# Performance work log

Measured on AMD Instinct MI355X. Metric: run time of the kernel, lower is better.

The kernel has to match this reference:

```python
import jax, jax.numpy as jnp
import numpy as np
from jax import lax

B, C_IN, C_OUT, T, D = 8, 32, 32, 2048, 32
L = T + 1  # max_timesteps=2048 is even -> pos length 2049


def setup_inputs() -> dict:
    key = jax.random.key(0)
    ks = jax.random.split(key, 8)
    x = jax.random.normal(ks[0], (B, C_IN, T), dtype=jnp.float32)
    # register_buffer pos_rel = linspace(-1, 1, L) with shape (1, 1, L)
    pos_rel = jnp.linspace(-1.0, 1.0, L, dtype=jnp.float32).reshape(1, 1, L)
    # SIREN init: first Conv1d weight ~ U(-1,1); later layers ~ U(-val,val), val=sqrt(6/in)/omega_0 (omega_0=1)
    w1 = jax.random.uniform(ks[1], (D, 1), jnp.float32, -1.0, 1.0)
    b1 = jax.random.uniform(ks[2], (D,), jnp.float32, -1.0, 1.0)
    val2 = float(np.sqrt(6.0 / D))
    w2 = jax.random.uniform(ks[3], (D, D), jnp.float32, -val2, val2)
    b2 = jax.random.uniform(ks[4], (D,), jnp.float32, -val2, val2)
    w3 = jax.random.uniform(ks[5], (C_OUT * C_IN, D), jnp.float32, -val2, val2)
    b3 = jax.random.uniform(ks[6], (C_OUT * C_IN,), jnp.float32, -val2, val2)
    bias = jax.random.normal(ks[7], (C_OUT,), dtype=jnp.float32)
    return {"x": x, "pos_rel": pos_rel, "w1": w1, "b1": b1, "w2": w2,
            "b2": b2, "w3": w3, "b3": b3, "bias": bias}


def reference(x, pos_rel, w1, b1, w2, b2, w3, b3, bias):
    # Kernel network (all kernel_size-1 convs == pointwise matmuls over positions).
    # Note: Sine.forward is sin(linear(x)); omega_0 param is unused in forward.
    p = pos_rel[0]                                   # (1, L)
    h = jnp.sin(w1 @ p + b1[:, None])                # (D, L)
    h = jnp.sin(w2 @ h + b2[:, None])                # (D, L)
    k = w3 @ h + b3[:, None]                         # (C_OUT*C_IN, L)
    kernel = k.reshape(C_OUT, C_IN, L)               # conv weight (O, I, K)
    # Causal left-padding with K-1 zeros, then VALID cross-correlation (torch conv1d semantics).
    xp = jnp.pad(x, ((0, 0), (0, 0), (L - 1, 0)))    # (B, C_IN, T+L-1)
    out = lax.conv_general_dilated(xp, kernel, window_strides=(1,), padding='VALID',
                                   dimension_numbers=('NCH', 'OIH', 'NCH'))
    return out + bias[None, :, None]                 # (B, C_OUT, T)
```

## Files before the change

kernel.cpp:

```cpp
#include <hip/hip_runtime.h>
#include <hip/hip_bf16.h>

#define BATCH 8
#define TLEN 2048
#define PADR 256
#define XT_ROWS (TLEN + PADR + 64)
#define GT_BYTES (2048*1024*2)
#define XT_BYTES (BATCH*XT_ROWS*32*2)
#define PART_OFF ((GT_BYTES + XT_BYTES + 255) & ~255)
#define JOBS_PER_B 144
#define NJOBS (BATCH*JOBS_PER_B)

using short8 = __attribute__((ext_vector_type(8))) short;
using f32x4  = __attribute__((ext_vector_type(4))) float;

typedef __attribute__((address_space(3))) char lds_char;
typedef __attribute__((address_space(1))) const char g_char;
static __device__ __forceinline__ void gload16(const void* g, void* l) {
    __builtin_amdgcn_global_load_lds((g_char*)g, (lds_char*)l, 16, 0, 0);
}

__global__ __launch_bounds__(256) void prep_kernel(
        const float* __restrict__ pos, const float* __restrict__ w1,
        const float* __restrict__ b1, const float* __restrict__ w2,
        const float* __restrict__ b2, const float* __restrict__ w3,
        const float* __restrict__ b3, const float* __restrict__ x,
        __hip_bfloat16* __restrict__ Gt, __hip_bfloat16* __restrict__ xT) {
    __shared__ float ot[128][65];
    int tid = threadIdx.x;
    if (blockIdx.x < 256) {
        int dblk = blockIdx.x >> 3, oblk = blockIdx.x & 7;
        int l  = tid & 63;
        int wu = __builtin_amdgcn_readfirstlane(tid >> 6);
        int d  = dblk*64 + l;
        float p = pos[2048 - d];
        float t1[32], h2[32];
        #pragma unroll
        for (int k = 0; k < 32; ++k) t1[k] = sinf(w1[k]*p + b1[k]);
        #pragma unroll
        for (int j = 0; j < 32; ++j) {
            float s0 = 0.f, s1 = 0.f;
            #pragma unroll
            for (int k = 0; k < 16; ++k) {
                s0 += w2[j*32 + k]      * t1[k];
                s1 += w2[j*32 + 16 + k] * t1[16 + k];
            }
            h2[j] = sinf(b2[j] + s0 + s1);
        }
        int obase = oblk*128 + wu*32;
        for (int ji = 0; ji < 32; ++ji) {
            int oi = obase + ji;
            float s0 = 0.f, s1 = 0.f;
            #pragma unroll
            for (int k = 0; k < 16; ++k) {
                s0 += w3[oi*32 + k]      * h2[k];
                s1 += w3[oi*32 + 16 + k] * h2[16 + k];
            }
            ot[wu*32 + ji][l] = b3[oi] + s0 + s1;
        }
        __syncthreads();
        #pragma unroll
        for (int it = 0; it < 32; ++it) {
            int e  = it*256 + tid;
            int dl = e >> 7, jq = e & 127;
            Gt[(size_t)(dblk*64 + dl)*1024 + oblk*128 + jq] = __float2bfloat16(ot[jq][dl]);
        }
    } else {
        int blk = blockIdx.x - 256;
        int b = blk >> 5;
        int c = blk & 31;
        int t0 = c * 64;
        #pragma unroll
        for (int r = 0; r < 8; ++r) {
            int i  = r*4 + (tid >> 6);
            int tl = tid & 63;
            ot[i][tl] = x[((size_t)(b*32 + i))*TLEN + t0 + tl];
        }
        __syncthreads();
        #pragma unroll
        for (int r = 0; r < 8; ++r) {
            int idx = r*256 + tid;
            int tl = idx >> 5, i = idx & 31;
            xT[((size_t)(b*XT_ROWS + PADR + t0 + tl))*32 + i] = __float2bfloat16(ot[i][tl]);
        }
        if (c == 0) {
            for (int idx = tid; idx < PADR*32; idx += 256)
                xT[(size_t)b*XT_ROWS*32 + idx] = __float2bfloat16(0.0f);
        }
        if (c == 1) {
            for (int idx = tid; idx < 64*32; idx += 256)
                xT[((size_t)b*XT_ROWS + PADR + TLEN)*32 + idx] = __float2bfloat16(0.0f);
        }
    }
}

#define MFMA8(A0,A1,A2,A3,B0,B1)                                                  \
    acc[0][0] = __builtin_amdgcn_mfma_f32_16x16x32_bf16(A0, B0, acc[0][0], 0,0,0); \
    acc[0][1] = __builtin_amdgcn_mfma_f32_16x16x32_bf16(A0, B1, acc[0][1], 0,0,0); \
    acc[1][0] = __builtin_amdgcn_mfma_f32_16x16x32_bf16(A1, B0, acc[1][0], 0,0,0); \
    acc[1][1] = __builtin_amdgcn_mfma_f32_16x16x32_bf16(A1, B1, acc[1][1], 0,0,0); \
    acc[2][0] = __builtin_amdgcn_mfma_f32_16x16x32_bf16(A2, B0, acc[2][0], 0,0,0); \
    acc[2][1] = __builtin_amdgcn_mfma_f32_16x16x32_bf16(A2, B1, acc[2][1], 0,0,0); \
    acc[3][0] = __builtin_amdgcn_mfma_f32_16x16x32_bf16(A3, B0, acc[3][0], 0,0,0); \
    acc[3][1] = __builtin_amdgcn_mfma_f32_16x16x32_bf16(A3, B1, acc[3][1], 0,0,0);

__global__ __launch_bounds__(256) void conv_mfma(const __hip_bfloat16* __restrict__ GtB,
                                                 const __hip_bfloat16* __restrict__ xTB,
                                                 float* __restrict__ partial) {
    __shared__ short8 lds_a[320*4];
    __shared__ short8 lds_b[2][1024];
    int tid  = threadIdx.x;
    int lane = tid & 63;
    int wu   = __builtin_amdgcn_readfirstlane(tid >> 6);
    int jid  = blockIdx.x;
    int b    = jid / JOBS_PER_B;
    int r    = jid - b * JOBS_PER_B;
    int J = (int)((sqrtf(2.0f*r + 1.0f) - 1.0f) * 0.5f);
    while (2*(J+1)*(J+2) <= r) ++J;
    while (2*J*(J+1) > r) --J;
    int S  = r - 2*J*(J+1);
    int d0 = 64*S;

    const short8* xs = (const short8*)xTB;
    int g0 = b*XT_ROWS + PADR + 256*J - 64*S - 63;
    #pragma unroll
    for (int c = 0; c < 5; ++c) {
        int lr   = c*64 + (tid >> 2);
        int slot = tid & 3;
        lds_a[lr*4 + (slot ^ ((lr >> 1) & 3))] = xs[(size_t)(g0 + lr)*4 + slot];
    }
    const char* gB = (const char*)GtB + (size_t)d0*2048;
    {
        const char* src = gB + wu*4096 + lane*16;
        char*       dst = (char*)(&lds_b[0][0]) + wu*4096;
        #pragma unroll
        for (int i = 0; i < 4; ++i) gload16(src + i*1024, dst + i*1024);
    }
    __syncthreads();

    int l15 = lane & 15, l4 = lane >> 4;
    int r0 = 63 + 64*wu + l15;

    f32x4 acc[4][2];
    const f32x4 zero = {0.f, 0.f, 0.f, 0.f};
    #pragma unroll
    for (int mt = 0; mt < 4; ++mt) { acc[mt][0] = zero; acc[mt][1] = zero; }

    for (int p = 0; p < 8; ++p) {
        if (p < 7) {
            const char* src = gB + (p+1)*16384 + wu*4096 + lane*16;
            char*       dst = (char*)(&lds_b[(p+1)&1][0]) + wu*4096;
            #pragma unroll
            for (int i = 0; i < 4; ++i) gload16(src + i*1024, dst + i*1024);
        }
        const short8* bb = &lds_b[p&1][0];
        #pragma unroll
        for (int q = 0; q < 8; ++q) {
            short8 bv0 = bb[q*128 + l15*4 + l4];
            short8 bv1 = bb[q*128 + l15*4 + l4 + 64];
            int ai = r0*4 + (l4 ^ ((r0 >> 1) & 3));
            short8 a0 = lds_a[ai], a1 = lds_a[ai+64], a2 = lds_a[ai+128], a3 = lds_a[ai+192];
            r0--;
            MFMA8(a0, a1, a2, a3, bv0, bv1)
        }
        __syncthreads();
    }

    float* pw = partial + (size_t)jid * 8192;
    #pragma unroll
    for (int no = 0; no < 2; ++no)
        #pragma unroll
        for (int mt = 0; mt < 4; ++mt) {
            int addr = (16*no + l15)*256 + 64*wu + 16*mt + l4*4;
            *reinterpret_cast<f32x4*>(pw + addr) = acc[mt][no];
        }
}

__global__ void reduce_out(const float* __restrict__ partial, const float* __restrict__ bias,
                           float* __restrict__ out) {
    int gid = blockIdx.x * 256 + threadIdx.x;
    int tl = gid & 255;
    int J  = (gid >> 8) & 7;
    int o  = (gid >> 11) & 31;
    int b  = gid >> 16;
    int jid = b*JOBS_PER_B + 2*J*(J+1);
    int cnt = 4*(J+1);
    const float* p = partial + (size_t)jid*8192 + o*256 + tl;
    float s0 = 0.f, s1 = 0.f, s2 = 0.f, s3 = 0.f;
    for (int sg = 0; sg < cnt; sg += 4) {
        s0 += p[(size_t)sg*8192];
        s1 += p[(size_t)(sg+1)*8192];
        s2 += p[(size_t)(sg+2)*8192];
        s3 += p[(size_t)(sg+3)*8192];
    }
    out[((size_t)(b*32 + o))*TLEN + 256*J + tl] = bias[o] + ((s0 + s1) + (s2 + s3));
}

extern "C" void kernel_launch(void* const* d_in, const int* in_sizes, int n_in,
                              void* d_out, int out_size, void* d_ws, size_t ws_size,
                              hipStream_t stream) {
    const float* x    = (const float*)d_in[0];
    const float* pos  = (const float*)d_in[1];
    const float* w1   = (const float*)d_in[2];
    const float* b1   = (const float*)d_in[3];
    const float* w2   = (const float*)d_in[4];
    const float* b2   = (const float*)d_in[5];
    const float* w3   = (const float*)d_in[6];
    const float* b3   = (const float*)d_in[7];
    const float* bias = (const float*)d_in[8];
    float* out = (float*)d_out;

    char* ws = (char*)d_ws;
    __hip_bfloat16* Gt = (__hip_bfloat16*)ws;
    __hip_bfloat16* xT = (__hip_bfloat16*)(ws + GT_BYTES);
    float* partial     = (float*)(ws + PART_OFF);

    hipLaunchKernelGGL(prep_kernel, dim3(512),   dim3(256), 0, stream,
                       pos, w1, b1, w2, b2, w3, b3, x, Gt, xT);
    hipLaunchKernelGGL(conv_mfma,   dim3(NJOBS), dim3(256), 0, stream, Gt, xT, partial);
    hipLaunchKernelGGL(reduce_out,  dim3(2048),  dim3(256), 0, stream, partial, bias, out);
}
```

Before: 151.1 us.

## Replace partial-sum buffer and reduce kernel with atomic accumulation into output

```diff
diff --git a/kernel.cpp b/kernel.cpp
--- a/kernel.cpp
+++ b/kernel.cpp
@@ -7,7 +7,6 @@
 #define XT_ROWS (TLEN + PADR + 64)
 #define GT_BYTES (2048*1024*2)
 #define XT_BYTES (BATCH*XT_ROWS*32*2)
-#define PART_OFF ((GT_BYTES + XT_BYTES + 255) & ~255)
 #define JOBS_PER_B 144
 #define NJOBS (BATCH*JOBS_PER_B)
 
@@ -25,7 +24,9 @@
         const float* __restrict__ b1, const float* __restrict__ w2,
         const float* __restrict__ b2, const float* __restrict__ w3,
         const float* __restrict__ b3, const float* __restrict__ x,
-        __hip_bfloat16* __restrict__ Gt, __hip_bfloat16* __restrict__ xT) {
+        const float* __restrict__ bias,
+        __hip_bfloat16* __restrict__ Gt, __hip_bfloat16* __restrict__ xT,
+        float* __restrict__ out) {
     __shared__ float ot[128][65];
     int tid = threadIdx.x;
     if (blockIdx.x < 256) {
@@ -65,7 +66,7 @@
             int dl = e >> 7, jq = e & 127;
             Gt[(size_t)(dblk*64 + dl)*1024 + oblk*128 + jq] = __float2bfloat16(ot[jq][dl]);
         }
-    } else {
+    } else if (blockIdx.x < 512) {
         int blk = blockIdx.x - 256;
         int b = blk >> 5;
         int c = blk & 31;
@@ -91,6 +92,13 @@
             for (int idx = tid; idx < 64*32; idx += 256)
                 xT[((size_t)b*XT_ROWS + PADR + TLEN)*32 + idx] = __float2bfloat16(0.0f);
         }
+    } else {
+        int idx4 = (blockIdx.x - 512)*256 + tid;
+        int e    = idx4*4;
+        int o    = (e >> 11) & 31;
+        float bv = bias[o];
+        f32x4 v = {bv, bv, bv, bv};
+        *reinterpret_cast<f32x4*>(out + e) = v;
     }
 }
 
@@ -106,7 +114,7 @@
 
 __global__ __launch_bounds__(256) void conv_mfma(const __hip_bfloat16* __restrict__ GtB,
                                                  const __hip_bfloat16* __restrict__ xTB,
-                                                 float* __restrict__ partial) {
+                                                 float* __restrict__ out) {
     __shared__ short8 lds_a[320*4];
     __shared__ short8 lds_b[2][1024];
     int tid  = threadIdx.x;
@@ -166,34 +174,17 @@
         __syncthreads();
     }
 
-    float* pw = partial + (size_t)jid * 8192;
+    float* po = out + ((size_t)b*32)*TLEN + 256*J;
     #pragma unroll
     for (int no = 0; no < 2; ++no)
         #pragma unroll
         for (int mt = 0; mt < 4; ++mt) {
-            int addr = (16*no + l15)*256 + 64*wu + 16*mt + l4*4;
-            *reinterpret_cast<f32x4*>(pw + addr) = acc[mt][no];
-        }
-}
-
-__global__ void reduce_out(const float* __restrict__ partial, const float* __restrict__ bias,
-                           float* __restrict__ out) {
-    int gid = blockIdx.x * 256 + threadIdx.x;
-    int tl = gid & 255;
-    int J  = (gid >> 8) & 7;
-    int o  = (gid >> 11) & 31;
-    int b  = gid >> 16;
-    int jid = b*JOBS_PER_B + 2*J*(J+1);
-    int cnt = 4*(J+1);
-    const float* p = partial + (size_t)jid*8192 + o*256 + tl;
-    float s0 = 0.f, s1 = 0.f, s2 = 0.f, s3 = 0.f;
-    for (int sg = 0; sg < cnt; sg += 4) {
-        s0 += p[(size_t)sg*8192];
-        s1 += p[(size_t)(sg+1)*8192];
-        s2 += p[(size_t)(sg+2)*8192];
-        s3 += p[(size_t)(sg+3)*8192];
-    }
-    out[((size_t)(b*32 + o))*TLEN + 256*J + tl] = bias[o] + ((s0 + s1) + (s2 + s3));
+            int o  = 16*no + l15;
+            int tl = 64*wu + 16*mt + l4*4;
+            #pragma unroll
+            for (int jj = 0; jj < 4; ++jj)
+                atomicAdd(po + (size_t)o*TLEN + tl + jj, acc[mt][no][jj]);
+        }
 }
 
 extern "C" void kernel_launch(void* const* d_in, const int* in_sizes, int n_in,
@@ -213,10 +204,8 @@
     char* ws = (char*)d_ws;
     __hip_bfloat16* Gt = (__hip_bfloat16*)ws;
     __hip_bfloat16* xT = (__hip_bfloat16*)(ws + GT_BYTES);
-    float* partial     = (float*)(ws + PART_OFF);
-
-    hipLaunchKernelGGL(prep_kernel, dim3(512),   dim3(256), 0, stream,
-                       pos, w1, b1, w2, b2, w3, b3, x, Gt, xT);
-    hipLaunchKernelGGL(conv_mfma,   dim3(NJOBS), dim3(256), 0, stream, Gt, xT, partial);
-    hipLaunchKernelGGL(reduce_out,  dim3(2048),  dim3(256), 0, stream, partial, bias, out);
-}
+
+    hipLaunchKernelGGL(prep_kernel, dim3(1024), dim3(256), 0, stream,
+                       pos, w1, b1, w2, b2, w3, b3, x, bias, Gt, xT, out);
+    hipLaunchKernelGGL(conv_mfma,   dim3(NJOBS), dim3(256), 0, stream, Gt, xT, out);
+}
```

Result: slower. 279.8 us (+85.2%).
